# Kernel tuning notes

Measured on AMD Instinct MI355X. Metric: run time of the kernel, lower is better.

Reference implementation:

```python
import jax, jax.numpy as jnp
import numpy as np

BATCH = 8192
IN_CH = 64          # input_channels
CH = 256            # output channels per row
BOARD = 27          # board_edge**3
EDGE = 3
ROWS = 49           # 3*(board_edge+1)**2 + 1


def _wincon_mats():
    # Faithful port of init_wincon_matrix(); returns (27, 3, 49) 0/1 matrix.
    step = [0]
    mats = np.zeros((BOARD, EDGE, ROWS), dtype=np.float32)
    col = 0
    x = y = z = 0

    def put():
        mats[x + 3 * y + 9 * z, step[0], col] = 1
        step[0] = (step[0] + 1) % 3

    for x in range(3):
        for y in range(3):
            for z in range(3):
                put()
            col += 1
        for z in range(3):
            for y in range(3):
                put()
            col += 1
        for y in range(3):
            z = y
            put()
        col += 1
        for y in range(3):
            z = 2 - y
            put()
        col += 1
    for z in range(3):
        for y in range(3):
            for x in range(3):
                put()
            col += 1
        for y in range(3):
            x = y
            put()
        col += 1
        for y in range(3):
            x = 2 - y
            put()
        col += 1
    for y in range(3):
        for z in range(3):
            x = z
            put()
        col += 1
        for z in range(3):
            x = 2 - z
            put()
        col += 1
    for x in range(3):
        y = z = x
        put()
    col += 1
    for x in range(3):
        y = z = 2 - x
        put()
    col += 1
    for x in range(3):
        y = x
        z = 2 - x
        put()
    col += 1
    for x in range(3):
        z = x
        y = 2 - x
        put()
    col += 1
    return mats


_MATS = jnp.asarray(_wincon_mats())  # (board_size=27, edge=3, row_count=49)


def setup_inputs() -> dict:
    key = jax.random.key(0)
    k1, k2, k3 = jax.random.split(key, 3)
    x = jax.random.normal(k1, (BATCH, IN_CH * BOARD), dtype=jnp.float32)
    # keras 'random_normal' initializer: stddev 0.05
    v = jax.random.normal(k2, (EDGE, IN_CH, ROWS, CH), dtype=jnp.float32) * 0.05
    b = jax.random.normal(k3, (CH * ROWS,), dtype=jnp.float32) * 0.05
    return {"x": x, "v": v, "b": b}


def reference(x, v, b):
    # Weight synthesis: w[bd, i, r, c] = sum_e mats[bd, e, r] * v[e, i, r, c]
    # (same math as the broadcast+multiply+reduce in the original, fused via einsum)
    w = jnp.einsum('ber,eirc->birc', _MATS, v)            # (27, in_ch, 49, ch)
    w = w.reshape(BOARD * IN_CH, ROWS * CH)              # (1728, 12544)
    return x @ w + b
```

## Files before the change

### kernel.cpp

```cpp
#include <hip/hip_runtime.h>
#include <cstdint>
#include <cstddef>


#define XCOLS   1728
#define ROWS_W  49
#define KTOT    192
#define OUTW    12544
#define XELEMS  (8192 * XCOLS)

typedef __attribute__((ext_vector_type(8))) short short8;
typedef __attribute__((ext_vector_type(4))) float f32x4;

struct CellTab { int c[ROWS_W][3]; };

constexpr CellTab make_cells() {
    CellTab t{};
    int step = 0, col = 0;
    int x = 0, y = 0, z = 0;
#define PUT() do { t.c[col][step] = x + 3*y + 9*z; step = (step + 1) % 3; } while (0)
    for (x = 0; x < 3; ++x) {
        for (y = 0; y < 3; ++y) {
            for (z = 0; z < 3; ++z) PUT();
            ++col;
        }
        for (z = 0; z < 3; ++z) {
            for (y = 0; y < 3; ++y) PUT();
            ++col;
        }
        for (y = 0; y < 3; ++y) { z = y; PUT(); }
        ++col;
        for (y = 0; y < 3; ++y) { z = 2 - y; PUT(); }
        ++col;
    }
    for (z = 0; z < 3; ++z) {
        for (y = 0; y < 3; ++y) {
            for (x = 0; x < 3; ++x) PUT();
            ++col;
        }
        for (y = 0; y < 3; ++y) { x = y; PUT(); }
        ++col;
        for (y = 0; y < 3; ++y) { x = 2 - y; PUT(); }
        ++col;
    }
    for (y = 0; y < 3; ++y) {
        for (z = 0; z < 3; ++z) { x = z; PUT(); }
        ++col;
        for (z = 0; z < 3; ++z) { x = 2 - z; PUT(); }
        ++col;
    }
    for (x = 0; x < 3; ++x) { y = x; z = x; PUT(); }
    ++col;
    for (x = 0; x < 3; ++x) { y = 2 - x; z = 2 - x; PUT(); }
    ++col;
    for (x = 0; x < 3; ++x) { y = x; z = 2 - x; PUT(); }
    ++col;
    for (x = 0; x < 3; ++x) { z = x; y = 2 - x; PUT(); }
    ++col;
#undef PUT
    return t;
}

__constant__ CellTab CELLS = make_cells();

__device__ __forceinline__ unsigned short f2bf(float f) {
    union { float f; unsigned u; } a; a.f = f;
    unsigned u = a.u;
    return (unsigned short)((u + 0x7fffu + ((u >> 16) & 1u)) >> 16);
}

__global__ __launch_bounds__(256) void x_prepass(const float* __restrict__ x,
                                                 unsigned short* __restrict__ xb) {
    const size_t i8 = (size_t)(blockIdx.x * 256 + threadIdx.x) * 8;
    const float4 a0 = *(const float4*)(x + i8);
    const float4 a1 = *(const float4*)(x + i8 + 4);
    short8 s;
    s[0] = (short)f2bf(a0.x); s[1] = (short)f2bf(a0.y);
    s[2] = (short)f2bf(a0.z); s[3] = (short)f2bf(a0.w);
    s[4] = (short)f2bf(a1.x); s[5] = (short)f2bf(a1.y);
    s[6] = (short)f2bf(a1.z); s[7] = (short)f2bf(a1.w);
    *(short8*)(xb + i8) = s;
}

__global__ __launch_bounds__(256) void wt_prepass(const float* __restrict__ v,
                                                  unsigned short* __restrict__ wt) {
    const int kq = blockIdx.x;
    const int r  = blockIdx.y;
    const int c  = threadIdx.x;
    const int k0 = kq * 32;
    unsigned short tmp[32];
#pragma unroll
    for (int kk = 0; kk < 32; ++kk) {
        const int k = k0 + kk;
        tmp[kk] = f2bf(v[(size_t)(k * 49 + r) * 256 + c]);
    }
    unsigned short* dst = wt + (size_t)(r * 256 + c) * KTOT + k0;
#pragma unroll
    for (int j = 0; j < 4; ++j) {
        short8 s;
#pragma unroll
        for (int i = 0; i < 8; ++i) s[i] = (short)tmp[j * 8 + i];
        *(short8*)(dst + j * 8) = s;
    }
}

__global__ __launch_bounds__(256, 2) void tic_gemm(
    const unsigned short* __restrict__ xb,
    const unsigned short* __restrict__ wt,
    const float* __restrict__ bias,
    float* __restrict__ out)
{
    const int bid   = blockIdx.x;
    const int m     = bid / 49;
    const int r     = bid % 49;
    const int mbase = m * 128;

    const int t    = threadIdx.x;
    const int wave = t >> 6;
    const int lane = t & 63;
    const int l15  = lane & 15;
    const int quad = lane >> 4;
    const int half = wave & 1;
    const int wh   = wave >> 1;

    __shared__ __align__(16) unsigned short Bs[2][8192];

    const int cells[3] = { CELLS.c[r][0], CELLS.c[r][1], CELLS.c[r][2] };

    f32x4 acc[4][8];
#pragma unroll
    for (int nt = 0; nt < 8; ++nt) {
        const float bv = bias[r * 256 + half * 128 + nt * 16 + l15];
        f32x4 a; a[0] = bv; a[1] = bv; a[2] = bv; a[3] = bv;
#pragma unroll
        for (int mt = 0; mt < 4; ++mt) acc[mt][nt] = a;
    }

    auto stageB = [&](int kc, int buf) {
#pragma unroll
        for (int q = 0; q < 4; ++q) {
            const int cb = q * 256 + wave * 64;
            const int n  = wave * 64 + lane;
            const unsigned short* src =
                wt + (size_t)(r * 256 + n) * KTOT + kc * 32 + q * 8;
            unsigned short* dst = &Bs[buf][cb * 8];
            __builtin_amdgcn_global_load_lds(
                (const __attribute__((address_space(1))) unsigned int*)src,
                (__attribute__((address_space(3))) unsigned int*)dst,
                16, 0, 0);
        }
    };

    short8 afr[2][4];
    auto loadA = [&](int kc, int parity) {
        const int e = kc >> 1, h = kc & 1;
        const int colb = cells[e] * 64 + h * 32 + quad * 8;
#pragma unroll
        for (int mt = 0; mt < 4; ++mt) {
            const int row = mbase + wh * 64 + mt * 16 + l15;
            afr[parity][mt] = *(const short8*)(xb + (size_t)row * XCOLS + colb);
        }
    };

    loadA(0, 0);
    stageB(0, 0);
    __syncthreads();

#pragma unroll
    for (int kc = 0; kc < 6; ++kc) {
        const int buf = kc & 1;
        if (kc < 5) {
            stageB(kc + 1, buf ^ 1);
            loadA(kc + 1, (kc + 1) & 1);
        }
#pragma unroll
        for (int nt = 0; nt < 8; ++nt) {
            const short8 bfr = *(const short8*)
                &Bs[buf][(quad * 256 + half * 128 + nt * 16 + l15) * 8];
#pragma unroll
            for (int mt = 0; mt < 4; ++mt)
                acc[mt][nt] = __builtin_amdgcn_mfma_f32_16x16x32_bf16(
                    afr[kc & 1][mt], bfr, acc[mt][nt], 0, 0, 0);
        }
        __syncthreads();
    }

#pragma unroll
    for (int mt = 0; mt < 4; ++mt) {
#pragma unroll
        for (int v4 = 0; v4 < 4; ++v4) {
            const int row = mbase + wh * 64 + mt * 16 + quad * 4 + v4;
            float* orow = out + (size_t)row * OUTW + r * 256 + half * 128;
#pragma unroll
            for (int nt = 0; nt < 8; ++nt)
                orow[nt * 16 + l15] = acc[mt][nt][v4];
        }
    }
}

extern "C" void kernel_launch(void* const* d_in, const int* in_sizes, int n_in,
                              void* d_out, int out_size, void* d_ws, size_t ws_size,
                              hipStream_t stream) {
    const float* x  = (const float*)d_in[0];
    const float* v  = (const float*)d_in[1];
    const float* b  = (const float*)d_in[2];
    float* out = (float*)d_out;

    unsigned short* xb = (unsigned short*)d_ws;
    unsigned short* wt = xb + (size_t)XELEMS;

    x_prepass<<<dim3(XELEMS / (256 * 8)), dim3(256), 0, stream>>>(x, xb);
    wt_prepass<<<dim3(6, 49), dim3(256), 0, stream>>>(v, wt);
    tic_gemm<<<dim3(64 * 49), dim3(256), 0, stream>>>(xb, wt, b, out);
}
```

Before: 530.2 us.

## Load B fragments directly from global in MFMA layout, drop LDS staging

The weight prepass now writes bf16 weights in a fragment-ordered layout (r, kc, q, n, 8), so each lane can load its MFMA B operand straight from global memory with 16-byte loads. The GEMM kernel drops the LDS double buffer and all __syncthreads, double-buffering the B fragments in registers instead. This removes LDS traffic and barriers, but every wave now reads B from global/L2 itself, and the extra 16 short8 registers may raise register pressure and cut occupancy.

```diff
diff --git a/kernel.cpp b/kernel.cpp
--- a/kernel.cpp
+++ b/kernel.cpp
@@ -84,23 +84,18 @@
 
 __global__ __launch_bounds__(256) void wt_prepass(const float* __restrict__ v,
                                                   unsigned short* __restrict__ wt) {
-    const int kq = blockIdx.x;
+    const int kc = blockIdx.x;
     const int r  = blockIdx.y;
     const int c  = threadIdx.x;
-    const int k0 = kq * 32;
-    unsigned short tmp[32];
-#pragma unroll
-    for (int kk = 0; kk < 32; ++kk) {
-        const int k = k0 + kk;
-        tmp[kk] = f2bf(v[(size_t)(k * 49 + r) * 256 + c]);
-    }
-    unsigned short* dst = wt + (size_t)(r * 256 + c) * KTOT + k0;
-#pragma unroll
-    for (int j = 0; j < 4; ++j) {
+#pragma unroll
+    for (int q = 0; q < 4; ++q) {
         short8 s;
 #pragma unroll
-        for (int i = 0; i < 8; ++i) s[i] = (short)tmp[j * 8 + i];
-        *(short8*)(dst + j * 8) = s;
+        for (int j = 0; j < 8; ++j) {
+            const int k = kc * 32 + q * 8 + j;
+            s[j] = (short)f2bf(v[(size_t)k * OUTW + r * 256 + c]);
+        }
+        *(short8*)(wt + ((((size_t)r * 6 + kc) * 4 + q) * 256 + c) * 8) = s;
     }
 }
 
@@ -123,8 +118,6 @@
     const int half = wave & 1;
     const int wh   = wave >> 1;
 
-    __shared__ __align__(16) unsigned short Bs[2][8192];
-
     const int cells[3] = { CELLS.c[r][0], CELLS.c[r][1], CELLS.c[r][2] };
 
     f32x4 acc[4][8];
@@ -136,53 +129,45 @@
         for (int mt = 0; mt < 4; ++mt) acc[mt][nt] = a;
     }
 
-    auto stageB = [&](int kc, int buf) {
-#pragma unroll
-        for (int q = 0; q < 4; ++q) {
-            const int cb = q * 256 + wave * 64;
-            const int n  = wave * 64 + lane;
-            const unsigned short* src =
-                wt + (size_t)(r * 256 + n) * KTOT + kc * 32 + q * 8;
-            unsigned short* dst = &Bs[buf][cb * 8];
-            __builtin_amdgcn_global_load_lds(
-                (const __attribute__((address_space(1))) unsigned int*)src,
-                (__attribute__((address_space(3))) unsigned int*)dst,
-                16, 0, 0);
-        }
-    };
+    const unsigned short* wbase =
+        wt + ((size_t)(r * 24 + quad) * 256 + half * 128 + l15) * 8;
 
     short8 afr[2][4];
-    auto loadA = [&](int kc, int parity) {
+    short8 bfr[2][8];
+
+    auto loadA = [&](int kc, int p) {
         const int e = kc >> 1, h = kc & 1;
         const int colb = cells[e] * 64 + h * 32 + quad * 8;
 #pragma unroll
         for (int mt = 0; mt < 4; ++mt) {
             const int row = mbase + wh * 64 + mt * 16 + l15;
-            afr[parity][mt] = *(const short8*)(xb + (size_t)row * XCOLS + colb);
+            afr[p][mt] = *(const short8*)(xb + (size_t)row * XCOLS + colb);
         }
     };
+    auto loadB = [&](int kc, int p) {
+        const unsigned short* src = wbase + (size_t)kc * 8192;
+#pragma unroll
+        for (int nt = 0; nt < 8; ++nt)
+            bfr[p][nt] = *(const short8*)(src + nt * 128);
+    };
 
     loadA(0, 0);
-    stageB(0, 0);
-    __syncthreads();
+    loadB(0, 0);
 
 #pragma unroll
     for (int kc = 0; kc < 6; ++kc) {
-        const int buf = kc & 1;
+        const int p = kc & 1;
         if (kc < 5) {
-            stageB(kc + 1, buf ^ 1);
-            loadA(kc + 1, (kc + 1) & 1);
+            loadB(kc + 1, p ^ 1);
+            loadA(kc + 1, p ^ 1);
         }
 #pragma unroll
         for (int nt = 0; nt < 8; ++nt) {
-            const short8 bfr = *(const short8*)
-                &Bs[buf][(quad * 256 + half * 128 + nt * 16 + l15) * 8];
 #pragma unroll
             for (int mt = 0; mt < 4; ++mt)
                 acc[mt][nt] = __builtin_amdgcn_mfma_f32_16x16x32_bf16(
-                    afr[kc & 1][mt], bfr, acc[mt][nt], 0, 0, 0);
-        }
-        __syncthreads();
+                    afr[p][mt], bfr[p][nt], acc[mt][nt], 0, 0, 0);
+        }
     }
 
 #pragma unroll
```

Measured after the change: 511.7 us. 3.5% less time.
